# Performance work log

Hardware: AMD Instinct MI355X
Metric: run time of the kernel (lower is better)

## Reference

```python
import jax, jax.numpy as jnp
import numpy as np

EPS = 1e-5


def _bn(h, gamma, beta):
    # BatchNorm1d in training mode: batch statistics over node dim
    mu = h.mean(axis=0)
    var = h.var(axis=0)
    return gamma * (h - mu) * jax.lax.rsqrt(var + EPS) + beta


def _rgcn_layer(x, src, dst, etype, W, Wloop, b, n_dst):
    # Relation-specific gather-transform-scatter (DGL RelGraphConv, sum agg,
    # self-loop + bias, no regularizer).
    x_src = x[src]                                   # [E, in] gather
    num_rels = W.shape[0]
    m = jnp.zeros((x_src.shape[0], W.shape[2]), x.dtype)
    for r in range(num_rels):                        # small fixed relation count
        m = m + jnp.where((etype == r)[:, None], x_src @ W[r], 0.0)
    agg = jax.ops.segment_sum(m, dst, num_segments=n_dst)  # scatter-add to dst
    # DGL block convention: dst nodes are the prefix of src nodes
    return agg + x[:n_dst] @ Wloop + b


def setup_inputs() -> dict:
    key = jax.random.key(0)
    ks = jax.random.split(key, 16)
    N_SRC, N_DST0, N_DST1 = 200000, 50000, 10000
    E0, E1, R, H, C = 800000, 160000, 5, 256, 153
    s = 1.0 / np.sqrt(H)
    inp = {
        "x": jax.random.normal(ks[0], (N_SRC, H), jnp.float32),
        "src0": jax.random.randint(ks[1], (E0,), 0, N_SRC, jnp.int32),
        "dst0": jax.random.randint(ks[2], (E0,), 0, N_DST0, jnp.int32),
        "etype0": jax.random.randint(ks[3], (E0,), 0, R, jnp.int32),
        "src1": jax.random.randint(ks[4], (E1,), 0, N_DST0, jnp.int32),
        "dst1": jax.random.randint(ks[5], (E1,), 0, N_DST1, jnp.int32),
        "etype1": jax.random.randint(ks[6], (E1,), 0, R, jnp.int32),
        "n_dst0": N_DST0,
        "n_dst1": N_DST1,
        "W0": jax.random.normal(ks[7], (R, H, H), jnp.float32) * s,
        "Wl0": jax.random.normal(ks[8], (H, H), jnp.float32) * s,
        "b0": jnp.zeros((H,), jnp.float32),
        "g0": jnp.ones((H,), jnp.float32),
        "be0": jnp.zeros((H,), jnp.float32),
        "W1": jax.random.normal(ks[9], (R, H, H), jnp.float32) * s,
        "Wl1": jax.random.normal(ks[10], (H, H), jnp.float32) * s,
        "b1": jnp.zeros((H,), jnp.float32),
        "g1": jnp.ones((H,), jnp.float32),
        "be1": jnp.zeros((H,), jnp.float32),
        "Wm1": jax.random.normal(ks[11], (H, H), jnp.float32) * s,
        "bm1": jnp.zeros((H,), jnp.float32),
        "gm": jnp.ones((H,), jnp.float32),
        "bem": jnp.zeros((H,), jnp.float32),
        "Wm2": jax.random.normal(ks[12], (H, C), jnp.float32) * s,
        "bm2": jnp.zeros((C,), jnp.float32),
    }
    return inp


def reference(x, src0, dst0, etype0, src1, dst1, etype1, n_dst0, n_dst1,
              W0, Wl0, b0, g0, be0, W1, Wl1, b1, g1, be1,
              Wm1, bm1, gm, bem, Wm2, bm2):
    # layer 0
    h = _rgcn_layer(x, src0, dst0, etype0, W0, Wl0, b0, n_dst0)
    h = jax.nn.elu(_bn(h, g0, be0))
    # layer 1
    h = _rgcn_layer(h, src1, dst1, etype1, W1, Wl1, b1, n_dst1)
    h = jax.nn.elu(_bn(h, g1, be1))
    # MLP head (dropout is identity in eval)
    h = jax.nn.relu(_bn(h @ Wm1 + bm1, gm, bem))
    return h @ Wm2 + bm2
```

## Files before the change

kernel.cpp:

```cpp
#include <hip/hip_runtime.h>
#include <hip/hip_bf16.h>


#define HD   256
#define EPS  1e-5f
#define NREL 5
#define ND0  50000
#define ND1  10000
#define BK   64

typedef unsigned short ushort_t;
using f32x4  = __attribute__((ext_vector_type(4))) float;
using short8 = __attribute__((ext_vector_type(8))) short;

__device__ __forceinline__ ushort_t f2b(float f) {
    union { float f; unsigned u; } x; x.f = f;
    unsigned r = x.u + 0x7FFF + ((x.u >> 16) & 1);
    return (ushort_t)(r >> 16);
}
__device__ __forceinline__ float b2f(ushort_t h) {
    union { unsigned u; float f; } x; x.u = ((unsigned)h) << 16;
    return x.f;
}

#define GLOAD_LDS16(gp, lp)                                                     \
    __builtin_amdgcn_global_load_lds(                                           \
        (const __attribute__((address_space(1))) unsigned int*)(gp),            \
        (__attribute__((address_space(3))) unsigned int*)(lp), 16, 0, 0)

struct WconvArgs {
    const float* src[14];
    ushort_t*    dst[14];
    int          N[14];
};
__global__ void wconv_all_kernel(WconvArgs a) {
    int mat = blockIdx.x >> 8;
    int id = (blockIdx.x & 255) * 256 + threadIdx.x;
    int n = id >> 8, k = id & 255;
    int N = a.N[mat];
    float v = (n < N) ? a.src[mat][(size_t)k * N + n] : 0.f;
    a.dst[mat][id] = f2b(v);
}

__global__ void xconv_kernel(const float* __restrict__ x, ushort_t* __restrict__ xb,
                             int n4) {
    int id = blockIdx.x * 256 + threadIdx.x;
    if (id >= n4) return;
    float4 v = ((const float4*)x)[id];
    ushort4 o; o.x = f2b(v.x); o.y = f2b(v.y); o.z = f2b(v.z); o.w = f2b(v.w);
    ((ushort4*)xb)[id] = o;
}

__global__ void count2_kernel(const int* __restrict__ d0, const int* __restrict__ e0, int E0,
                              const int* __restrict__ d1, const int* __restrict__ e1, int E1,
                              int* __restrict__ cnt, int* __restrict__ pos) {
    int e = blockIdx.x * 256 + threadIdx.x;
    if (e < E0) {
        pos[e] = atomicAdd(&cnt[e0[e] * ND0 + d0[e]], 1);
    } else if (e < E0 + E1) {
        int i = e - E0;
        pos[e] = atomicAdd(&cnt[NREL * ND0 + e1[i] * ND1 + d1[i]], 1);
    }
}

__global__ void scan_block_kernel(const int* __restrict__ in, int* __restrict__ out,
                                  int* __restrict__ bsum, int nb) {
    __shared__ int ts[256];
    int tid = threadIdx.x;
    int base = blockIdx.x * 1024 + tid * 4;
    int v0 = (base + 0 < nb) ? in[base + 0] : 0;
    int v1 = (base + 1 < nb) ? in[base + 1] : 0;
    int v2 = (base + 2 < nb) ? in[base + 2] : 0;
    int v3 = (base + 3 < nb) ? in[base + 3] : 0;
    int tsum = v0 + v1 + v2 + v3;
    ts[tid] = tsum;
    __syncthreads();
    for (int d = 1; d < 256; d <<= 1) {
        int t = (tid >= d) ? ts[tid - d] : 0;
        __syncthreads();
        ts[tid] += t;
        __syncthreads();
    }
    int excl = ts[tid] - tsum;
    if (base + 0 < nb) out[base + 0] = excl;
    if (base + 1 < nb) out[base + 1] = excl + v0;
    if (base + 2 < nb) out[base + 2] = excl + v0 + v1;
    if (base + 3 < nb) out[base + 3] = excl + v0 + v1 + v2;
    if (tid == 255 && bsum) bsum[blockIdx.x] = ts[255];
}

__global__ void scan_add_kernel(int* __restrict__ out, const int* __restrict__ bsum, int nb) {
    int i = blockIdx.x * 256 + threadIdx.x;
    if (i < nb) out[i] += bsum[i >> 10];
}

__global__ void fill2_kernel(const int* __restrict__ s0, const int* __restrict__ d0,
                             const int* __restrict__ e0, int E0,
                             const int* __restrict__ s1, const int* __restrict__ d1,
                             const int* __restrict__ e1, int E1,
                             const int* __restrict__ pos, const int* __restrict__ off,
                             int* __restrict__ ssrc) {
    int e = blockIdx.x * 256 + threadIdx.x;
    if (e < E0) {
        ssrc[off[e0[e] * ND0 + d0[e]] + pos[e]] = s0[e];
    } else if (e < E0 + E1) {
        int i = e - E0;
        ssrc[off[NREL * ND0 + e1[i] * ND1 + d1[i]] + pos[e]] = s1[i];
    }
}

__global__ void gather_kernel(const ushort_t* __restrict__ feat, const int* __restrict__ ssrc,
                              const int* __restrict__ cnt, const int* __restrict__ off,
                              int nbuckets, ushort_t* __restrict__ out,
                              const float* __restrict__ sc, const float* __restrict__ sh) {
    int wave = (blockIdx.x * 256 + threadIdx.x) >> 6;
    int lane = threadIdx.x & 63;
    if (wave >= nbuckets) return;
    int deg = cnt[wave], s = off[wave];
    float4 scv = {0, 0, 0, 0}, shv = {0, 0, 0, 0};
    if (sc) { scv = ((const float4*)sc)[lane]; shv = ((const float4*)sh)[lane]; }
    float a0 = 0, a1 = 0, a2 = 0, a3 = 0;
    if (sc) {
        for (int j = 0; j < deg; j++) {
            ushort4 v = ((const ushort4*)(feat + (size_t)ssrc[s + j] * HD))[lane];
            float f0 = fmaf(b2f(v.x), scv.x, shv.x);
            float f1 = fmaf(b2f(v.y), scv.y, shv.y);
            float f2 = fmaf(b2f(v.z), scv.z, shv.z);
            float f3 = fmaf(b2f(v.w), scv.w, shv.w);
            a0 += f0 > 0.f ? f0 : expm1f(f0);
            a1 += f1 > 0.f ? f1 : expm1f(f1);
            a2 += f2 > 0.f ? f2 : expm1f(f2);
            a3 += f3 > 0.f ? f3 : expm1f(f3);
        }
    } else {
        int j = 0;
        for (; j + 2 <= deg; j += 2) {
            int r0 = ssrc[s + j], r1 = ssrc[s + j + 1];
            ushort4 v0 = ((const ushort4*)(feat + (size_t)r0 * HD))[lane];
            ushort4 v1 = ((const ushort4*)(feat + (size_t)r1 * HD))[lane];
            a0 += b2f(v0.x) + b2f(v1.x); a1 += b2f(v0.y) + b2f(v1.y);
            a2 += b2f(v0.z) + b2f(v1.z); a3 += b2f(v0.w) + b2f(v1.w);
        }
        if (j < deg) {
            ushort4 v = ((const ushort4*)(feat + (size_t)ssrc[s + j] * HD))[lane];
            a0 += b2f(v.x); a1 += b2f(v.y); a2 += b2f(v.z); a3 += b2f(v.w);
        }
    }
    ushort4 o; o.x = f2b(a0); o.y = f2b(a1); o.z = f2b(a2); o.w = f2b(a3);
    ((ushort4*)(out + (size_t)wave * HD))[lane] = o;
}

__global__ void bnprep_kernel(const float* __restrict__ sums, const float* __restrict__ g,
                              const float* __restrict__ be, float invM,
                              float* __restrict__ sc, float* __restrict__ sh) {
    int c = threadIdx.x;
    float mu = sums[c] * invM;
    float var = sums[HD + c] * invM - mu * mu;
    float s = g[c] * rsqrtf(var + EPS);
    sc[c] = s; sh[c] = be[c] - mu * s;
}

struct Seg {
    const ushort_t* A;
    const ushort_t* B;
    const float* sc;
    const float* sh;
    int act;
};
struct GemmArgs {
    Seg seg[6];
    int nseg;
    const float* bias;
    float* stats;
    ushort_t* Cb;
    float* Cf;
    int M, N;
};

template <int BM>
__launch_bounds__(256, 4)
__global__ void gemm_mfma_kernel(GemmArgs g) {
    constexpr int F   = BM / 32;
    constexpr int NFT = BM / 16;
    constexpr int IT  = NFT * 2 / 4;
    __shared__ __align__(1024) ushort_t As[NFT * 2 * 512];
    __shared__ __align__(1024) ushort_t Bs[NFT * 2 * 512];
    int tid = threadIdx.x;
    int wave = tid >> 6, lane = tid & 63;
    int rq = lane >> 4, ci = lane & 15;
    int wm = (wave >> 1) * (BM / 2), wn = (wave & 1) * (BM / 2);
    int bm = blockIdx.y * BM, bn = blockIdx.x * BM;
    f32x4 acc[F][F] = {};
    int K = g.nseg * HD;

    for (int kk = 0; kk < K; kk += BK) {
        int si = kk >> 8;
        int kl = kk & 255;
        const ushort_t* Ap = g.seg[si].A;
        const ushort_t* Bp = g.seg[si].B;
        const float* sc = g.seg[si].sc;
        if (!sc) {
#pragma unroll
            for (int it = 0; it < IT; it++) {
                int f = it * 4 + wave;
                int mt = f >> 1, kt = f & 1;
                const ushort_t* ga = Ap + (size_t)(bm + mt * 16 + ci) * HD
                                        + kl + kt * 32 + rq * 8;
                GLOAD_LDS16(ga, &As[f * 512 + lane * 8]);
            }
        } else {
            const float* sh = g.seg[si].sh;
            int act = g.seg[si].act;
#pragma unroll
            for (int it = 0; it < IT; it++) {
                int f = it * 4 + wave;
                int mt = f >> 1, kt = f & 1;
                int kb = kl + kt * 32 + rq * 8;
                uint4 v = *(const uint4*)(Ap + (size_t)(bm + mt * 16 + ci) * HD + kb);
                ushort_t* u = (ushort_t*)&v;
#pragma unroll
                for (int j = 0; j < 8; j++) {
                    float fv = fmaf(b2f(u[j]), sc[kb + j], sh[kb + j]);
                    fv = (act == 2) ? fmaxf(fv, 0.f) : (fv > 0.f ? fv : expm1f(fv));
                    u[j] = f2b(fv);
                }
                *(uint4*)&As[f * 512 + lane * 8] = v;
            }
        }
#pragma unroll
        for (int it = 0; it < IT; it++) {
            int f = it * 4 + wave;
            int nt = f >> 1, kt = f & 1;
            const ushort_t* gb = Bp + (size_t)(bn + nt * 16 + ci) * HD
                                    + kl + kt * 32 + rq * 8;
            GLOAD_LDS16(gb, &Bs[f * 512 + lane * 8]);
        }
        __syncthreads();
#pragma unroll
        for (int ks = 0; ks < 2; ks++) {
            short8 a[F], b[F];
#pragma unroll
            for (int mi = 0; mi < F; mi++)
                a[mi] = *(const short8*)&As[((wm / 16 + mi) * 2 + ks) * 512 + lane * 8];
#pragma unroll
            for (int ni = 0; ni < F; ni++)
                b[ni] = *(const short8*)&Bs[((wn / 16 + ni) * 2 + ks) * 512 + lane * 8];
#pragma unroll
            for (int mi = 0; mi < F; mi++)
#pragma unroll
                for (int ni = 0; ni < F; ni++)
                    acc[mi][ni] = __builtin_amdgcn_mfma_f32_16x16x32_bf16(
                        a[mi], b[ni], acc[mi][ni], 0, 0, 0);
        }
        __syncthreads();
    }

#pragma unroll
    for (int ni = 0; ni < F; ni++) {
        int col = bn + wn + ni * 16 + ci;
        float bv = (col < g.N) ? g.bias[col] : 0.f;
#pragma unroll
        for (int mi = 0; mi < F; mi++)
#pragma unroll
            for (int reg = 0; reg < 4; reg++) acc[mi][ni][reg] += bv;
    }
    if (g.stats) {
#pragma unroll
        for (int ni = 0; ni < F; ni++) {
            float s = 0.f, s2 = 0.f;
#pragma unroll
            for (int mi = 0; mi < F; mi++)
#pragma unroll
                for (int reg = 0; reg < 4; reg++) {
                    int row = bm + wm + mi * 16 + rq * 4 + reg;
                    if (row < g.M) { float v = acc[mi][ni][reg]; s += v; s2 += v * v; }
                }
            s  += __shfl_xor(s, 16);  s  += __shfl_xor(s, 32);
            s2 += __shfl_xor(s2, 16); s2 += __shfl_xor(s2, 32);
            if (rq == 0) {
                int col = bn + wn + ni * 16 + ci;
                atomicAdd(&g.stats[col], s);
                atomicAdd(&g.stats[HD + col], s2);
            }
        }
    }
#pragma unroll
    for (int mi = 0; mi < F; mi++)
#pragma unroll
        for (int ni = 0; ni < F; ni++)
#pragma unroll
            for (int reg = 0; reg < 4; reg++) {
                int row = bm + wm + mi * 16 + rq * 4 + reg;
                int col = bn + wn + ni * 16 + ci;
                if (row < g.M && col < g.N) {
                    float v = acc[mi][ni][reg];
                    if (g.Cb) g.Cb[(size_t)row * HD + col] = f2b(v);
                    else      g.Cf[(size_t)row * g.N + col] = v;
                }
            }
}

extern "C" void kernel_launch(void* const* d_in, const int* in_sizes, int n_in,
                              void* d_out, int out_size, void* d_ws, size_t ws_size,
                              hipStream_t stream) {
    const float* x   = (const float*)d_in[0];
    const int* src0  = (const int*)d_in[1];
    const int* dst0  = (const int*)d_in[2];
    const int* et0   = (const int*)d_in[3];
    const int* src1  = (const int*)d_in[4];
    const int* dst1  = (const int*)d_in[5];
    const int* et1   = (const int*)d_in[6];
    const float* W0  = (const float*)d_in[9];
    const float* Wl0 = (const float*)d_in[10];
    const float* b0  = (const float*)d_in[11];
    const float* g0  = (const float*)d_in[12];
    const float* be0 = (const float*)d_in[13];
    const float* W1  = (const float*)d_in[14];
    const float* Wl1 = (const float*)d_in[15];
    const float* b1  = (const float*)d_in[16];
    const float* g1  = (const float*)d_in[17];
    const float* be1 = (const float*)d_in[18];
    const float* Wm1 = (const float*)d_in[19];
    const float* bm1 = (const float*)d_in[20];
    const float* gm  = (const float*)d_in[21];
    const float* bem = (const float*)d_in[22];
    const float* Wm2 = (const float*)d_in[23];
    const float* bm2 = (const float*)d_in[24];

    const int E0 = in_sizes[1];
    const int E1 = in_sizes[4];
    const int NOUT = in_sizes[24];
    const int NSRC = in_sizes[0] / HD;
    const int NBKT = NREL * ND0 + NREL * ND1;

    char* p = (char*)d_ws;
    ushort_t* Wt = (ushort_t*)p;  p += (size_t)14 * 65536 * 2;
    float* st    = (float*)p;     p += 1536 * 4;
    float* bnp   = (float*)p;     p += 6 * 256 * 4;
    int* cnt     = (int*)p;       p += (size_t)NBKT * 4;
    int* off     = (int*)p;       p += (size_t)NBKT * 4;
    int* bsum    = (int*)p;       p += 1024 * 4;
    int* pos     = (int*)p;       p += (size_t)(E0 + E1) * 4;
    int* ssrc    = (int*)p;       p += (size_t)(E0 + E1) * 4;
    ushort_t* xb  = (ushort_t*)p; p += (size_t)NSRC * HD * 2;
    ushort_t* S0  = (ushort_t*)p; p += (size_t)(NREL * ND0 + 128) * HD * 2;
    ushort_t* S1  = (ushort_t*)p; p += (size_t)(NREL * ND1 + 128) * HD * 2;
    ushort_t* h0b = (ushort_t*)p; p += (size_t)(ND0 + 128) * HD * 2;
    ushort_t* h1b = (ushort_t*)p; p += (size_t)(ND1 + 128) * HD * 2;
    ushort_t* mb  = (ushort_t*)p; p += (size_t)(ND1 + 128) * HD * 2;

    float* st0 = st, *st1 = st + 512, *stm = st + 1024;
    float* sc0 = bnp, *sh0 = bnp + 256, *sc1 = bnp + 512, *sh1 = bnp + 768;
    float* scm = bnp + 1024, *shm = bnp + 1280;

    ushort_t* W0t  = Wt;
    ushort_t* Wl0t = Wt + 5 * 65536;
    ushort_t* W1t  = Wt + 6 * 65536;
    ushort_t* Wl1t = Wt + 11 * 65536;
    ushort_t* Wm1t = Wt + 12 * 65536;
    ushort_t* Wm2t = Wt + 13 * 65536;

    {
        WconvArgs wa;
        for (int r = 0; r < NREL; r++) { wa.src[r] = W0 + (size_t)r * 65536; wa.dst[r] = W0t + (size_t)r * 65536; wa.N[r] = 256; }
        wa.src[5] = Wl0; wa.dst[5] = Wl0t; wa.N[5] = 256;
        for (int r = 0; r < NREL; r++) { wa.src[6 + r] = W1 + (size_t)r * 65536; wa.dst[6 + r] = W1t + (size_t)r * 65536; wa.N[6 + r] = 256; }
        wa.src[11] = Wl1; wa.dst[11] = Wl1t; wa.N[11] = 256;
        wa.src[12] = Wm1; wa.dst[12] = Wm1t; wa.N[12] = 256;
        wa.src[13] = Wm2; wa.dst[13] = Wm2t; wa.N[13] = NOUT;
        wconv_all_kernel<<<14 * 256, 256, 0, stream>>>(wa);
    }
    xconv_kernel<<<(NSRC * 64 + 255) / 256, 256, 0, stream>>>(x, xb, NSRC * 64);
    hipMemsetAsync(st, 0, 1536 * sizeof(float), stream);
    hipMemsetAsync(cnt, 0, (size_t)NBKT * sizeof(int), stream);

    int ET = E0 + E1;
    count2_kernel<<<(ET + 255) / 256, 256, 0, stream>>>(dst0, et0, E0, dst1, et1, E1, cnt, pos);
    int nsb = (NBKT + 1023) / 1024;
    scan_block_kernel<<<nsb, 256, 0, stream>>>(cnt, off, bsum, NBKT);
    scan_block_kernel<<<1, 256, 0, stream>>>(bsum, bsum, nullptr, nsb);
    scan_add_kernel<<<(NBKT + 255) / 256, 256, 0, stream>>>(off, bsum, NBKT);
    fill2_kernel<<<(ET + 255) / 256, 256, 0, stream>>>(src0, dst0, et0, E0, src1, dst1, et1, E1, pos, off, ssrc);

    gather_kernel<<<(NREL * ND0 * 64) / 256, 256, 0, stream>>>(
        xb, ssrc, cnt, off, NREL * ND0, S0, nullptr, nullptr);
    {
        GemmArgs ga = {};
        for (int s = 0; s < NREL; s++)
            ga.seg[s] = { S0 + (size_t)s * ND0 * HD, W0t + (size_t)s * 65536, nullptr, nullptr, 0 };
        ga.seg[5] = { xb, Wl0t, nullptr, nullptr, 0 };
        ga.nseg = 6; ga.bias = b0; ga.stats = st0;
        ga.Cb = h0b; ga.Cf = nullptr; ga.M = ND0; ga.N = HD;
        gemm_mfma_kernel<128><<<dim3(2, (ND0 + 127) / 128), 256, 0, stream>>>(ga);
    }
    bnprep_kernel<<<1, 256, 0, stream>>>(st0, g0, be0, 1.f / ND0, sc0, sh0);

    gather_kernel<<<(NREL * ND1 * 64) / 256, 256, 0, stream>>>(
        h0b, ssrc, cnt + NREL * ND0, off + NREL * ND0, NREL * ND1, S1, sc0, sh0);
    {
        GemmArgs ga = {};
        for (int s = 0; s < NREL; s++)
            ga.seg[s] = { S1 + (size_t)s * ND1 * HD, W1t + (size_t)s * 65536, nullptr, nullptr, 0 };
        ga.seg[5] = { h0b, Wl1t, sc0, sh0, 1 };
        ga.nseg = 6; ga.bias = b1; ga.stats = st1;
        ga.Cb = h1b; ga.Cf = nullptr; ga.M = ND1; ga.N = HD;
        gemm_mfma_kernel<64><<<dim3(4, (ND1 + 63) / 64), 256, 0, stream>>>(ga);
    }
    bnprep_kernel<<<1, 256, 0, stream>>>(st1, g1, be1, 1.f / ND1, sc1, sh1);

    {
        GemmArgs ga = {};
        ga.seg[0] = { h1b, Wm1t, sc1, sh1, 1 };
        ga.nseg = 1; ga.bias = bm1; ga.stats = stm;
        ga.Cb = mb; ga.Cf = nullptr; ga.M = ND1; ga.N = HD;
        gemm_mfma_kernel<64><<<dim3(4, (ND1 + 63) / 64), 256, 0, stream>>>(ga);
    }
    bnprep_kernel<<<1, 256, 0, stream>>>(stm, gm, bem, 1.f / ND1, scm, shm);
    {
        GemmArgs ga = {};
        ga.seg[0] = { mb, Wm2t, scm, shm, 2 };
        ga.nseg = 1; ga.bias = bm2; ga.stats = nullptr;
        ga.Cb = nullptr; ga.Cf = (float*)d_out; ga.M = ND1; ga.N = NOUT;
        gemm_mfma_kernel<64><<<dim3((NOUT + 63) / 64, (ND1 + 63) / 64), 256, 0, stream>>>(ga);
    }
}
```

Baseline: 755.9 us.

## Double-buffer GEMM LDS tiles and unroll gather loops by four

The MFMA GEMM moves from a single-buffered BK=64 loop with two syncs per step to a double-buffered K=32 pipeline. The next tile's loads are issued before the current tile's MFMAs, leaving one barrier per step. The gather kernel now unrolls neighbor loads by four in both the plain and the BN+ELU paths, so more independent row loads are in flight. The trade-offs are twice as many k-iterations with less work each, and more registers used in the gather.

```diff
diff --git a/kernel.cpp b/kernel.cpp
--- a/kernel.cpp
+++ b/kernel.cpp
@@ -7,7 +7,6 @@
 #define NREL 5
 #define ND0  50000
 #define ND1  10000
-#define BK   64
 
 typedef unsigned short ushort_t;
 using f32x4  = __attribute__((ext_vector_type(4))) float;
@@ -109,6 +108,18 @@
     }
 }
 
+__device__ __forceinline__ void bnelu_acc(ushort4 v, const float4& scv, const float4& shv,
+                                          float& a0, float& a1, float& a2, float& a3) {
+    float f0 = fmaf(b2f(v.x), scv.x, shv.x);
+    float f1 = fmaf(b2f(v.y), scv.y, shv.y);
+    float f2 = fmaf(b2f(v.z), scv.z, shv.z);
+    float f3 = fmaf(b2f(v.w), scv.w, shv.w);
+    a0 += f0 > 0.f ? f0 : expm1f(f0);
+    a1 += f1 > 0.f ? f1 : expm1f(f1);
+    a2 += f2 > 0.f ? f2 : expm1f(f2);
+    a3 += f3 > 0.f ? f3 : expm1f(f3);
+}
+
 __global__ void gather_kernel(const ushort_t* __restrict__ feat, const int* __restrict__ ssrc,
                               const int* __restrict__ cnt, const int* __restrict__ off,
                               int nbuckets, ushort_t* __restrict__ out,
@@ -117,31 +128,42 @@
     int lane = threadIdx.x & 63;
     if (wave >= nbuckets) return;
     int deg = cnt[wave], s = off[wave];
-    float4 scv = {0, 0, 0, 0}, shv = {0, 0, 0, 0};
-    if (sc) { scv = ((const float4*)sc)[lane]; shv = ((const float4*)sh)[lane]; }
     float a0 = 0, a1 = 0, a2 = 0, a3 = 0;
     if (sc) {
-        for (int j = 0; j < deg; j++) {
+        float4 scv = ((const float4*)sc)[lane];
+        float4 shv = ((const float4*)sh)[lane];
+        int j = 0;
+        for (; j + 4 <= deg; j += 4) {
+            int r0 = ssrc[s + j + 0], r1 = ssrc[s + j + 1];
+            int r2 = ssrc[s + j + 2], r3 = ssrc[s + j + 3];
+            ushort4 v0 = ((const ushort4*)(feat + (size_t)r0 * HD))[lane];
+            ushort4 v1 = ((const ushort4*)(feat + (size_t)r1 * HD))[lane];
+            ushort4 v2 = ((const ushort4*)(feat + (size_t)r2 * HD))[lane];
+            ushort4 v3 = ((const ushort4*)(feat + (size_t)r3 * HD))[lane];
+            bnelu_acc(v0, scv, shv, a0, a1, a2, a3);
+            bnelu_acc(v1, scv, shv, a0, a1, a2, a3);
+            bnelu_acc(v2, scv, shv, a0, a1, a2, a3);
+            bnelu_acc(v3, scv, shv, a0, a1, a2, a3);
+        }
+        for (; j < deg; j++) {
             ushort4 v = ((const ushort4*)(feat + (size_t)ssrc[s + j] * HD))[lane];
-            float f0 = fmaf(b2f(v.x), scv.x, shv.x);
-            float f1 = fmaf(b2f(v.y), scv.y, shv.y);
-            float f2 = fmaf(b2f(v.z), scv.z, shv.z);
-            float f3 = fmaf(b2f(v.w), scv.w, shv.w);
-            a0 += f0 > 0.f ? f0 : expm1f(f0);
-            a1 += f1 > 0.f ? f1 : expm1f(f1);
-            a2 += f2 > 0.f ? f2 : expm1f(f2);
-            a3 += f3 > 0.f ? f3 : expm1f(f3);
+            bnelu_acc(v, scv, shv, a0, a1, a2, a3);
         }
     } else {
         int j = 0;
-        for (; j + 2 <= deg; j += 2) {
-            int r0 = ssrc[s + j], r1 = ssrc[s + j + 1];
+        for (; j + 4 <= deg; j += 4) {
+            int r0 = ssrc[s + j + 0], r1 = ssrc[s + j + 1];
+            int r2 = ssrc[s + j + 2], r3 = ssrc[s + j + 3];
             ushort4 v0 = ((const ushort4*)(feat + (size_t)r0 * HD))[lane];
             ushort4 v1 = ((const ushort4*)(feat + (size_t)r1 * HD))[lane];
-            a0 += b2f(v0.x) + b2f(v1.x); a1 += b2f(v0.y) + b2f(v1.y);
-            a2 += b2f(v0.z) + b2f(v1.z); a3 += b2f(v0.w) + b2f(v1.w);
-        }
-        if (j < deg) {
+            ushort4 v2 = ((const ushort4*)(feat + (size_t)r2 * HD))[lane];
+            ushort4 v3 = ((const ushort4*)(feat + (size_t)r3 * HD))[lane];
+            a0 += b2f(v0.x) + b2f(v1.x) + b2f(v2.x) + b2f(v3.x);
+            a1 += b2f(v0.y) + b2f(v1.y) + b2f(v2.y) + b2f(v3.y);
+            a2 += b2f(v0.z) + b2f(v1.z) + b2f(v2.z) + b2f(v3.z);
+            a3 += b2f(v0.w) + b2f(v1.w) + b2f(v2.w) + b2f(v3.w);
+        }
+        for (; j < deg; j++) {
             ushort4 v = ((const ushort4*)(feat + (size_t)ssrc[s + j] * HD))[lane];
             a0 += b2f(v.x); a1 += b2f(v.y); a2 += b2f(v.z); a3 += b2f(v.w);
         }
@@ -182,76 +204,77 @@
 __global__ void gemm_mfma_kernel(GemmArgs g) {
     constexpr int F   = BM / 32;
     constexpr int NFT = BM / 16;
-    constexpr int IT  = NFT * 2 / 4;
-    __shared__ __align__(1024) ushort_t As[NFT * 2 * 512];
-    __shared__ __align__(1024) ushort_t Bs[NFT * 2 * 512];
+    constexpr int IT  = NFT / 4;
+    __shared__ __align__(1024) ushort_t As[2][NFT * 512];
+    __shared__ __align__(1024) ushort_t Bs[2][NFT * 512];
     int tid = threadIdx.x;
     int wave = tid >> 6, lane = tid & 63;
     int rq = lane >> 4, ci = lane & 15;
     int wm = (wave >> 1) * (BM / 2), wn = (wave & 1) * (BM / 2);
+    int wmf = wm >> 4, wnf = wn >> 4;
     int bm = blockIdx.y * BM, bn = blockIdx.x * BM;
     f32x4 acc[F][F] = {};
     int K = g.nseg * HD;
-
-    for (int kk = 0; kk < K; kk += BK) {
-        int si = kk >> 8;
-        int kl = kk & 255;
+    int NT = K >> 5;
+
+    auto stage = [&](int b, int t) {
+        int k = t << 5;
+        int si = k >> 8;
+        int kl = k & 255;
         const ushort_t* Ap = g.seg[si].A;
         const ushort_t* Bp = g.seg[si].B;
         const float* sc = g.seg[si].sc;
         if (!sc) {
 #pragma unroll
             for (int it = 0; it < IT; it++) {
-                int f = it * 4 + wave;
-                int mt = f >> 1, kt = f & 1;
-                const ushort_t* ga = Ap + (size_t)(bm + mt * 16 + ci) * HD
-                                        + kl + kt * 32 + rq * 8;
-                GLOAD_LDS16(ga, &As[f * 512 + lane * 8]);
+                int mt = it * 4 + wave;
+                GLOAD_LDS16(Ap + (size_t)(bm + mt * 16 + ci) * HD + kl + rq * 8,
+                            &As[b][mt * 512 + lane * 8]);
             }
         } else {
             const float* sh = g.seg[si].sh;
             int act = g.seg[si].act;
+            int kb = kl + rq * 8;
 #pragma unroll
             for (int it = 0; it < IT; it++) {
-                int f = it * 4 + wave;
-                int mt = f >> 1, kt = f & 1;
-                int kb = kl + kt * 32 + rq * 8;
+                int mt = it * 4 + wave;
                 uint4 v = *(const uint4*)(Ap + (size_t)(bm + mt * 16 + ci) * HD + kb);
                 ushort_t* u = (ushort_t*)&v;
 #pragma unroll
-                for (int j = 0; j < 8; j++) {
-                    float fv = fmaf(b2f(u[j]), sc[kb + j], sh[kb + j]);
+                for (int jj = 0; jj < 8; jj++) {
+                    float fv = fmaf(b2f(u[jj]), sc[kb + jj], sh[kb + jj]);
                     fv = (act == 2) ? fmaxf(fv, 0.f) : (fv > 0.f ? fv : expm1f(fv));
-                    u[j] = f2b(fv);
+                    u[jj] = f2b(fv);
                 }
-                *(uint4*)&As[f * 512 + lane * 8] = v;
+                *(uint4*)&As[b][mt * 512 + lane * 8] = v;
             }
         }
 #pragma unroll
         for (int it = 0; it < IT; it++) {
-            int f = it * 4 + wave;
-            int nt = f >> 1, kt = f & 1;
-            const ushort_t* gb = Bp + (size_t)(bn + nt * 16 + ci) * HD
-                                    + kl + kt * 32 + rq * 8;
-            GLOAD_LDS16(gb, &Bs[f * 512 + lane * 8]);
-        }
-        __syncthreads();
-#pragma unroll
-        for (int ks = 0; ks < 2; ks++) {
-            short8 a[F], b[F];
-#pragma unroll
-            for (int mi = 0; mi < F; mi++)
-                a[mi] = *(const short8*)&As[((wm / 16 + mi) * 2 + ks) * 512 + lane * 8];
+            int nt = it * 4 + wave;
+            GLOAD_LDS16(Bp + (size_t)(bn + nt * 16 + ci) * HD + kl + rq * 8,
+                        &Bs[b][nt * 512 + lane * 8]);
+        }
+    };
+
+    stage(0, 0);
+    __syncthreads();
+    for (int t = 0; t < NT; t++) {
+        int cur = t & 1;
+        if (t + 1 < NT) stage(cur ^ 1, t + 1);
+        short8 a[F], b[F];
+#pragma unroll
+        for (int mi = 0; mi < F; mi++)
+            a[mi] = *(const short8*)&As[cur][(wmf + mi) * 512 + lane * 8];
+#pragma unroll
+        for (int ni = 0; ni < F; ni++)
+            b[ni] = *(const short8*)&Bs[cur][(wnf + ni) * 512 + lane * 8];
+#pragma unroll
+        for (int mi = 0; mi < F; mi++)
 #pragma unroll
             for (int ni = 0; ni < F; ni++)
-                b[ni] = *(const short8*)&Bs[((wn / 16 + ni) * 2 + ks) * 512 + lane * 8];
-#pragma unroll
-            for (int mi = 0; mi < F; mi++)
-#pragma unroll
-                for (int ni = 0; ni < F; ni++)
-                    acc[mi][ni] = __builtin_amdgcn_mfma_f32_16x16x32_bf16(
-                        a[mi], b[ni], acc[mi][ni], 0, 0, 0);
-        }
+                acc[mi][ni] = __builtin_amdgcn_mfma_f32_16x16x32_bf16(
+                    a[mi], b[ni], acc[mi][ni], 0, 0, 0);
         __syncthreads();
     }
 
```

New measurement: 774.4 us. 2.4% more time.
